# Performance work log

Hardware: AMD Instinct MI355X
Metric: run time of the kernel (lower is better)

## Reference

```python
import jax, jax.numpy as jnp
import numpy as np

H = 8          # num_channels (heads)
POS = 16       # pos_dim
MAX_F = 16.0
MIN_F = 1.0
HALF_S = 16    # samples_per_dim=32 -> offsets -16..16, S=33
SCALE = POS ** -0.5


def setup_inputs() -> dict:
    key = jax.random.key(0)
    ks = jax.random.split(key, 12)
    B, L, C = 2, 4096, 1024
    p = 0.02
    return {
        'x': jax.random.normal(ks[0], (B, L, C), jnp.float32),
        'wave_w': jax.random.normal(ks[1], (C, 3 * H), jnp.float32) * p,
        'wave_b': jax.random.normal(ks[2], (3 * H,), jnp.float32) * p,
        'query_w': jax.random.normal(ks[3], (C, H * POS), jnp.float32) * p,
        'query_b': jax.random.normal(ks[4], (H * POS,), jnp.float32) * p,
        'key_w': jax.random.normal(ks[5], (POS,), jnp.float32) * p,
        'out_w': jax.random.normal(ks[6], (C, C), jnp.float32) * p,
        'se1_w': jax.random.normal(ks[7], (C, C // 4), jnp.float32) * p,
        'se1_b': jax.random.normal(ks[8], (C // 4,), jnp.float32) * p,
        'se2_w': jax.random.normal(ks[9], (C // 4, C), jnp.float32) * p,
        'se2_b': jax.random.normal(ks[10], (C,), jnp.float32) * p,
    }


def _adaptive_conv(x, wave_w, wave_b, query_w, query_b, key_w, out_w,
                   se1_w, se1_b, se2_w, se2_b):
    B, L, C = x.shape
    D = C // H
    silu = jax.nn.silu
    offsets = jnp.arange(-HALF_S, HALF_S + 1, dtype=x.dtype)  # [S]
    S = offsets.shape[0]

    # wave params -> freq/phase/decay per (B,L,H)
    wave = silu(x @ wave_w + wave_b).reshape(B, L, 3, H)
    freq = jax.nn.sigmoid(wave[:, :, 0, :]) * (MAX_F - MIN_F) + MIN_F
    phase = jnp.tanh(wave[:, :, 1, :]) * MAX_F
    decay = jax.nn.sigmoid(wave[:, :, 2, :]) * 9.5 + 0.5
    queries = silu(x @ query_w + query_b).reshape(B, L, H, POS)

    freq_avg = freq.mean(axis=-1)    # [B,L]
    phase_avg = phase.mean(axis=-1)  # [B,L]

    centers = jnp.arange(L, dtype=x.dtype)
    # [B,L,S] real-valued sample positions
    sample_pos = (centers[None, :, None]
                  + offsets[None, None, :] * freq_avg[..., None]
                  + phase_avg[..., None])
    valid = (sample_pos >= 0) & (sample_pos < L)           # [B,L,S]
    sample_idx = jnp.clip(sample_pos.astype(jnp.int32), 0, L - 1)

    # gather: values[b,l,s,:] = x[b, sample_idx[b,l,s], :]
    values = jnp.take_along_axis(x, sample_idx.reshape(B, L * S, 1), axis=1)
    values = values.reshape(B, L, S, H, D).transpose(0, 1, 3, 2, 4)  # [B,L,H,S,D]

    rel = jnp.abs(offsets)[None, None, None, :] * freq[..., None]    # [B,L,H,S]
    keys = silu(rel[..., None] * key_w)                              # [B,L,H,S,POS]
    logits = jnp.einsum('blhd,blhsd->blhs', queries, keys) * SCALE

    vmask = valid[:, :, None, :]                                     # [B,L,H,S]
    logits = jnp.where(vmask, logits, -1e30)
    env = jnp.exp(-rel / jnp.maximum(decay[..., None], 0.1))
    w = jax.nn.softmax(logits, axis=-1) * env * vmask.astype(x.dtype)
    w = w / (w.sum(axis=-1, keepdims=True) + 1e-8)

    out = jnp.einsum('blhsd,blhs->blhd', values, w).reshape(B, L, C)
    se = jax.nn.sigmoid(silu(out @ se1_w + se1_b) @ se2_w + se2_b)
    out = out * se
    return silu(out @ out_w)


def reference(x, wave_w, wave_b, query_w, query_b, key_w, out_w,
              se1_w, se1_b, se2_w, se2_b):
    return _adaptive_conv(x, wave_w, wave_b, query_w, query_b, key_w,
                          out_w, se1_w, se1_b, se2_w, se2_b)
```

## Files before the change

kernel.cpp:

```cpp
#include <hip/hip_runtime.h>
#include <math.h>

#define HN 8
#define POSN 16
#define SN 33
#define HALF_SN 16
#define CDIM 1024
#define LDIM 4096
#define BDIM 2
#define NTOK (BDIM * LDIM)

typedef unsigned short u16;
typedef short short8 __attribute__((ext_vector_type(8)));
typedef u16 u16x8 __attribute__((ext_vector_type(8)));
typedef unsigned int u32x4 __attribute__((ext_vector_type(4)));
typedef float f32x4 __attribute__((ext_vector_type(4)));

__device__ __forceinline__ float sigf(float x) { return 1.0f / (1.0f + expf(-x)); }
__device__ __forceinline__ float siluf(float x) { return x / (1.0f + expf(-x)); }
__device__ __forceinline__ float frcp(float x) { return __builtin_amdgcn_rcpf(x); }
__device__ __forceinline__ float fexp(float x) { return __expf(x); }
__device__ __forceinline__ float fsig(float x) { return frcp(1.0f + fexp(-x)); }
__device__ __forceinline__ float fsilu(float x) { return x * fsig(x); }

__device__ __forceinline__ u16 f2b(float f) {
    union { float f; unsigned u; } v; v.f = f;
    unsigned r = v.u + 0x7fffu + ((v.u >> 16) & 1u);
    return (u16)(r >> 16);
}
__device__ __forceinline__ float b2f(u16 v) {
    union { unsigned u; float f; } x; x.u = ((unsigned)v) << 16; return x.f;
}
__device__ __forceinline__ float u2f(unsigned u) {
    union { unsigned u; float f; } x; x.u = u; return x.f;
}
__device__ __forceinline__ void ld_lds16(const void* g, void* l) {
    __builtin_amdgcn_global_load_lds(
        (const __attribute__((address_space(1))) void*)g,
        (__attribute__((address_space(3))) void*)l, 16, 0, 0);
}

__global__ __launch_bounds__(256) void transcast_all(
    const float* __restrict__ qw, const float* __restrict__ s1,
    const float* __restrict__ s2, const float* __restrict__ ow,
    const float* __restrict__ ww,
    u16* __restrict__ oq, u16* __restrict__ o1,
    u16* __restrict__ o2, u16* __restrict__ oo,
    float* __restrict__ owT)
{
    const int bid = blockIdx.x;
    if (bid >= 1664) {
        const int idx = (bid - 1664) * 256 + threadIdx.x;
        const int c = idx >> 10, k = idx & 1023;
        owT[idx] = ww[k * 24 + c];
        return;
    }
    const float* in; u16* out; int N, K, base;
    if      (bid < 128) { in = qw; out = oq; N = 128;  K = 1024; base = 0;   }
    else if (bid < 384) { in = s1; out = o1; N = 256;  K = 1024; base = 128; }
    else if (bid < 640) { in = s2; out = o2; N = 1024; K = 256;  base = 384; }
    else                { in = ow; out = oo; N = 1024; K = 1024; base = 640; }
    const int rel = bid - base, nx = N / 32;
    const int bn = (rel % nx) * 32, bk = (rel / nx) * 32;

    __shared__ float tile[32][33];
    const int tx = threadIdx.x & 31, ty = threadIdx.x >> 5;
    #pragma unroll
    for (int yy = ty; yy < 32; yy += 8)
        tile[yy][tx] = in[(size_t)(bk + yy) * N + bn + tx];
    __syncthreads();
    #pragma unroll
    for (int yy = ty; yy < 32; yy += 8)
        out[(size_t)(bn + yy) * K + bk + tx] = f2b(tile[tx][yy]);
}

__global__ __launch_bounds__(256) void wave_partial(
    const float* __restrict__ x, const float* __restrict__ wwT,
    u16* __restrict__ xbf, float* __restrict__ part)
{
    const int bid = blockIdx.x;
    const int sl = bid >> 7;
    const int tg = bid & 127;
    const int tid = threadIdx.x;
    const int t0 = tg * 64;
    const int k0 = sl * 128;

    __shared__ float wsct[24][128];

    for (int i = tid; i < 768; i += 256) {
        const int c = i >> 5, k4 = (i & 31) * 4;
        *(float4*)&wsct[c][k4] = *(const float4*)(wwT + (size_t)c * 1024 + k0 + k4);
    }
    for (int i = tid; i < 1024; i += 256) {
        const int r = i >> 4, c8 = (i & 15) * 8;
        const float* src = x + (size_t)(t0 + r) * CDIM + k0 + c8;
        float4 a = *(const float4*)(src);
        float4 b = *(const float4*)(src + 4);
        u16x8 o;
        o[0]=f2b(a.x); o[1]=f2b(a.y); o[2]=f2b(a.z); o[3]=f2b(a.w);
        o[4]=f2b(b.x); o[5]=f2b(b.y); o[6]=f2b(b.z); o[7]=f2b(b.w);
        *(u16x8*)(xbf + (size_t)(t0 + r) * CDIM + k0 + c8) = o;
    }
    __syncthreads();

    const int tok = tid & 63;
    const int cg  = tid >> 6;
    const int t = t0 + tok;
    const float* xr = x + (size_t)t * CDIM + k0;
    const int c0 = cg * 6;
    float a0=0.f, a1=0.f, a2=0.f, a3=0.f, a4=0.f, a5=0.f;

    #pragma unroll 4
    for (int kk = 0; kk < 128; kk += 4) {
        float4 xv = *(const float4*)(xr + kk);
        float4 w0 = *(const float4*)&wsct[c0 + 0][kk];
        float4 w1 = *(const float4*)&wsct[c0 + 1][kk];
        float4 w2 = *(const float4*)&wsct[c0 + 2][kk];
        float4 w3 = *(const float4*)&wsct[c0 + 3][kk];
        float4 w4 = *(const float4*)&wsct[c0 + 4][kk];
        float4 w5 = *(const float4*)&wsct[c0 + 5][kk];
        a0 += xv.x*w0.x; a0 += xv.y*w0.y; a0 += xv.z*w0.z; a0 += xv.w*w0.w;
        a1 += xv.x*w1.x; a1 += xv.y*w1.y; a1 += xv.z*w1.z; a1 += xv.w*w1.w;
        a2 += xv.x*w2.x; a2 += xv.y*w2.y; a2 += xv.z*w2.z; a2 += xv.w*w2.w;
        a3 += xv.x*w3.x; a3 += xv.y*w3.y; a3 += xv.z*w3.z; a3 += xv.w*w3.w;
        a4 += xv.x*w4.x; a4 += xv.y*w4.y; a4 += xv.z*w4.z; a4 += xv.w*w4.w;
        a5 += xv.x*w5.x; a5 += xv.y*w5.y; a5 += xv.z*w5.z; a5 += xv.w*w5.w;
    }
    float* pp = part + (size_t)sl * NTOK * 24 + (size_t)t * 24 + c0;
    pp[0]=a0; pp[1]=a1; pp[2]=a2; pp[3]=a3; pp[4]=a4; pp[5]=a5;
}

__global__ __launch_bounds__(256) void wave_fixup(
    const float* __restrict__ part, const float* __restrict__ wave_b,
    float* __restrict__ freq, float* __restrict__ decay,
    float* __restrict__ favg, float* __restrict__ pavg)
{
    const int tid = threadIdx.x;
    const int tok = tid >> 5, col = tid & 31;
    const int t = blockIdx.x * 8 + tok;
    __shared__ float fsh[8][9], psh[8][9];

    if (col < 24) {
        float s = wave_b[col];
        #pragma unroll
        for (int sl = 0; sl < 8; ++sl)
            s += part[(size_t)sl * NTOK * 24 + (size_t)t * 24 + col];
        const float val = siluf(s);
        if (col < 8) {
            float f = sigf(val) * 15.0f + 1.0f;
            freq[(size_t)t * HN + col] = f;
            fsh[tok][col] = f;
        } else if (col < 16) {
            psh[tok][col - 8] = tanhf(val) * 16.0f;
        } else {
            decay[(size_t)t * HN + (col - 16)] = sigf(val) * 9.5f + 0.5f;
        }
    }
    __syncthreads();
    if (col == 0) {
        float fa = 0.f, pa = 0.f;
        for (int h = 0; h < HN; ++h) { fa += fsh[tok][h]; pa += psh[tok][h]; }
        favg[t] = fa * 0.125f; pavg[t] = pa * 0.125f;
    }
}

template <int MODE, int CFG>
__global__ __launch_bounds__(256) void mfma_gemm(
    const u16* __restrict__ A, const u16* __restrict__ Bt,
    const float* __restrict__ bias, const u16* __restrict__ mulb,
    void* __restrict__ Cptr, int M, int N, int K)
{
    constexpr int BM  = (CFG == 0) ? 128 : 32;
    constexpr int MI  = (CFG == 0) ? 4 : 2;
    constexpr int NJ  = (CFG == 0) ? 4 : 2;
    constexpr int ACH = BM / 16;
    constexpr int NCH = ACH + 8;

    __shared__ u16 lds[2][(BM + 128) * 32];

    const int nwg = gridDim.x * gridDim.y;
    const int flat = blockIdx.y * gridDim.x + blockIdx.x;
    const int swz = (flat & 7) * (nwg >> 3) + (flat >> 3);
    const int bxi = swz / gridDim.y, byi = swz % gridDim.y;

    const int tid = threadIdx.x;
    const int bm = bxi * BM, bn = byi * 128;
    const int wid = tid >> 6, lane = tid & 63;
    const int wr = (CFG == 0) ? (wid >> 1) * 64 : 0;
    const int wc = (CFG == 0) ? (wid & 1) * 64 : wid * 32;
    const int fm = lane & 15;
    const int kg = (lane >> 4) * 8;
    const int lrow = lane >> 2;
    const int lk   = (lane & 3) * 8;

    f32x4 acc[MI][NJ];
    #pragma unroll
    for (int i = 0; i < MI; ++i)
        #pragma unroll
        for (int j = 0; j < NJ; ++j) acc[i][j] = (f32x4){0.f, 0.f, 0.f, 0.f};

    auto stage = [&](u16* dst, int k0s) {
        #pragma unroll
        for (int c = wid; c < NCH; c += 4) {
            const u16* gsrc = (c < ACH)
                ? A  + (size_t)(bm + c * 16 + lrow) * K + k0s + lk
                : Bt + (size_t)(bn + (c - ACH) * 16 + lrow) * K + k0s + lk;
            ld_lds16(gsrc, dst + c * 512 + lane * 8);
        }
    };

    stage(&lds[0][0], 0);
    __syncthreads();
    int cur = 0;
    for (int k0 = 0; k0 < K; k0 += 32) {
        const int k1 = (k0 + 32 < K) ? (k0 + 32) : k0;
        stage(&lds[cur ^ 1][0], k1);
        short8 a[MI], b[NJ];
        #pragma unroll
        for (int i = 0; i < MI; ++i)
            a[i] = *(const short8*)&lds[cur][(wr + i * 16 + fm) * 32 + kg];
        #pragma unroll
        for (int j = 0; j < NJ; ++j)
            b[j] = *(const short8*)&lds[cur][(BM + wc + j * 16 + fm) * 32 + kg];
        #pragma unroll
        for (int i = 0; i < MI; ++i)
            #pragma unroll
            for (int j = 0; j < NJ; ++j)
                acc[i][j] = __builtin_amdgcn_mfma_f32_16x16x32_bf16(a[i], b[j], acc[i][j], 0, 0, 0);
        __syncthreads();
        cur ^= 1;
    }

    float* Cf = (float*)Cptr;
    u16* Cb = (u16*)Cptr;
    #pragma unroll
    for (int i = 0; i < MI; ++i) {
        const int row0 = bm + wr + i * 16 + (lane >> 4) * 4;
        #pragma unroll
        for (int j = 0; j < NJ; ++j) {
            const int col = bn + wc + j * 16 + fm;
            const float vb = (MODE == 3) ? 0.0f : bias[col];
            #pragma unroll
            for (int e = 0; e < 4; ++e) {
                const int row = row0 + e;
                float v = acc[i][j][e];
                if (MODE == 1) v = fsilu(v + vb);
                if (MODE == 2) v = fsig(v + vb) * b2f(mulb[(size_t)row * N + col]);
                if (MODE == 3) v = fsilu(v);
                if (MODE == 3) Cf[(size_t)row * N + col] = v;
                else           Cb[(size_t)row * N + col] = f2b(v);
            }
        }
    }
}

__global__ __launch_bounds__(256) void adaptconv_kernel(
    const u16* __restrict__ xbf, const float* __restrict__ key_w,
    const u16* __restrict__ qb, const float* __restrict__ freq,
    const float* __restrict__ decay, const float* __restrict__ favg,
    const float* __restrict__ pavg, u16* __restrict__ out)
{
    const int bid = blockIdx.x;
    const int swz = (bid & 7) * (NTOK / 16) + (bid >> 3);
    const int sub = threadIdx.x >> 7, lt = threadIdx.x & 127;
    const int t = swz * 2 + sub;
    const int b = t / LDIM, l = t % LDIM;
    const int h = lt >> 4;
    const int li = lt & 15;

    __shared__ float qs[2][HN][17];
    __shared__ float kw[POSN];
    __shared__ float fr[2][HN], dc[2][HN];
    __shared__ int   boff[2][SN];
    __shared__ float msk[2][SN];
    __shared__ float vsh[2][HN][17];
    __shared__ float esh[2][HN][17];
    __shared__ float wgt[2][HN][SN];

    qs[sub][lt >> 4][lt & 15] = b2f(qb[(size_t)t * 128 + lt]);
    if (threadIdx.x < POSN) kw[threadIdx.x] = key_w[threadIdx.x];
    if (lt < HN) {
        fr[sub][lt] = freq[(size_t)t * HN + lt];
        dc[sub][lt] = decay[(size_t)t * HN + lt];
    }
    if (lt < SN) {
        float fa = favg[t], pa = pavg[t];
        float sp = (float)l + (float)(lt - HALF_SN) * fa + pa;
        bool v = (sp >= 0.0f) && (sp < (float)LDIM);
        int si = (int)sp;
        si = min(max(si, 0), LDIM - 1);
        boff[sub][lt] = si * (CDIM * 2);
        msk[sub][lt] = v ? 1.0f : 0.0f;
    }
    __syncthreads();

    {
        const float fh = fr[sub][h];
        const float rdci = frcp(fmaxf(dc[sub][h], 0.1f));
        for (int ds = li; ds < 17; ds += 16) {
            float rel = (float)ds * fh;
            float acc = 0.0f;
            #pragma unroll
            for (int p = 0; p < POSN; ++p)
                acc += qs[sub][h][p] * fsilu(rel * kw[p]);
            vsh[sub][h][ds] = 0.25f * acc;
            esh[sub][h][ds] = fexp(-rel * rdci);
        }
    }
    __syncthreads();

    {
        const int ns = (li == 0) ? 3 : 2;
        int   sI[3] = { li, li + 16, 32 };
        float lg[3];
        #pragma unroll
        for (int k = 0; k < 3; ++k) {
            if (k < ns) {
                const int s = sI[k], ds = abs(s - 16);
                lg[k] = (msk[sub][s] != 0.0f) ? vsh[sub][h][ds] : -1e30f;
            } else lg[k] = -3.4e38f;
        }
        float m = fmaxf(lg[0], fmaxf(lg[1], lg[2]));
        #pragma unroll
        for (int d = 1; d < 16; d <<= 1) m = fmaxf(m, __shfl_xor(m, d));

        float e[3]; float ssum = 0.0f;
        #pragma unroll
        for (int k = 0; k < 3; ++k) {
            e[k] = (k < ns) ? fexp(lg[k] - m) : 0.0f;
            ssum += e[k];
        }
        #pragma unroll
        for (int d = 1; d < 16; d <<= 1) ssum += __shfl_xor(ssum, d);

        const float rss = frcp(ssum);
        float wv[3]; float wsum = 0.0f;
        #pragma unroll
        for (int k = 0; k < 3; ++k) {
            if (k < ns) {
                const int s = sI[k], ds = abs(s - 16);
                wv[k] = e[k] * rss * esh[sub][h][ds] * msk[sub][s];
            } else wv[k] = 0.0f;
            wsum += wv[k];
        }
        #pragma unroll
        for (int d = 1; d < 16; d <<= 1) wsum += __shfl_xor(wsum, d);

        const float inv = frcp(wsum + 1e-8f);
        #pragma unroll
        for (int k = 0; k < 3; ++k)
            if (k < ns) wgt[sub][h][sI[k]] = wv[k] * inv;
    }
    __syncthreads();

    const char* xbB = (const char*)(xbf + (size_t)b * LDIM * CDIM);
    const int cbyte = lt * 16;
    float a0=0,a1=0,a2=0,a3=0,a4=0,a5=0,a6=0,a7=0;

    #define GFMA(V, W) do { \
        a0 += (W) * u2f((V)[0] << 16); a1 += (W) * u2f((V)[0] & 0xffff0000u); \
        a2 += (W) * u2f((V)[1] << 16); a3 += (W) * u2f((V)[1] & 0xffff0000u); \
        a4 += (W) * u2f((V)[2] << 16); a5 += (W) * u2f((V)[2] & 0xffff0000u); \
        a6 += (W) * u2f((V)[3] << 16); a7 += (W) * u2f((V)[3] & 0xffff0000u); } while (0)

    int s = 0;
    for (; s + 4 <= SN; s += 4) {
        u32x4 v0 = *(const u32x4*)(xbB + boff[sub][s]     + cbyte);
        u32x4 v1 = *(const u32x4*)(xbB + boff[sub][s + 1] + cbyte);
        u32x4 v2 = *(const u32x4*)(xbB + boff[sub][s + 2] + cbyte);
        u32x4 v3 = *(const u32x4*)(xbB + boff[sub][s + 3] + cbyte);
        float w0 = wgt[sub][h][s],     w1 = wgt[sub][h][s + 1];
        float w2 = wgt[sub][h][s + 2], w3 = wgt[sub][h][s + 3];
        GFMA(v0, w0); GFMA(v1, w1); GFMA(v2, w2); GFMA(v3, w3);
    }
    for (; s < SN; ++s) {
        u32x4 v = *(const u32x4*)(xbB + boff[sub][s] + cbyte);
        float w = wgt[sub][h][s];
        GFMA(v, w);
    }
    #undef GFMA

    u16x8 o;
    o[0]=f2b(a0); o[1]=f2b(a1); o[2]=f2b(a2); o[3]=f2b(a3);
    o[4]=f2b(a4); o[5]=f2b(a5); o[6]=f2b(a6); o[7]=f2b(a7);
    *(u16x8*)(out + (size_t)t * CDIM + lt * 8) = o;
}

extern "C" void kernel_launch(void* const* d_in, const int* in_sizes, int n_in,
                              void* d_out, int out_size, void* d_ws, size_t ws_size,
                              hipStream_t stream)
{
    const float* x       = (const float*)d_in[0];
    const float* wave_w  = (const float*)d_in[1];
    const float* wave_b  = (const float*)d_in[2];
    const float* query_w = (const float*)d_in[3];
    const float* query_b = (const float*)d_in[4];
    const float* key_w   = (const float*)d_in[5];
    const float* out_w   = (const float*)d_in[6];
    const float* se1_w   = (const float*)d_in[7];
    const float* se1_b   = (const float*)d_in[8];
    const float* se2_w   = (const float*)d_in[9];
    const float* se2_b   = (const float*)d_in[10];

    char* wsb = (char*)d_ws;
    u16* q_bf    = (u16*)wsb;           wsb += (size_t)NTOK * 128 * 2;
    float* freq  = (float*)wsb;         wsb += (size_t)NTOK * HN * 4;
    float* decay = (float*)wsb;         wsb += (size_t)NTOK * HN * 4;
    float* favg  = (float*)wsb;         wsb += (size_t)NTOK * 4;
    float* pavg  = (float*)wsb;         wsb += (size_t)NTOK * 4;
    u16* x_bf    = (u16*)wsb;           wsb += (size_t)NTOK * CDIM * 2;
    u16* conv_bf = (u16*)wsb;           wsb += (size_t)NTOK * CDIM * 2;
    u16* tmp1_bf = (u16*)wsb;           wsb += (size_t)NTOK * 256 * 2;
    u16* g_bf    = (u16*)wsb;           wsb += (size_t)NTOK * CDIM * 2;
    u16* qw_bf   = (u16*)wsb;           wsb += (size_t)128 * CDIM * 2;
    u16* se1w_bf = (u16*)wsb;           wsb += (size_t)256 * CDIM * 2;
    u16* se2w_bf = (u16*)wsb;           wsb += (size_t)CDIM * 256 * 2;
    u16* outw_bf = (u16*)wsb;           wsb += (size_t)CDIM * CDIM * 2;
    float* wwT   = (float*)wsb;         wsb += (size_t)24 * CDIM * 4;
    float* part  = (float*)wsb;         wsb += (size_t)8 * NTOK * 24 * 4;

    transcast_all<<<1760, 256, 0, stream>>>(
        query_w, se1_w, se2_w, out_w, wave_w,
        qw_bf, se1w_bf, se2w_bf, outw_bf, wwT);

    wave_partial<<<8 * 128, 256, 0, stream>>>(x, wwT, x_bf, part);
    wave_fixup<<<NTOK / 8, 256, 0, stream>>>(
        part, wave_b, freq, decay, favg, pavg);

    mfma_gemm<1, 1><<<dim3(NTOK / 32, 1), 256, 0, stream>>>(
        x_bf, qw_bf, query_b, nullptr, q_bf, NTOK, 128, CDIM);

    adaptconv_kernel<<<NTOK / 2, 256, 0, stream>>>(
        x_bf, key_w, q_bf, freq, decay, favg, pavg, conv_bf);

    mfma_gemm<1, 1><<<dim3(NTOK / 32, 256 / 128), 256, 0, stream>>>(
        conv_bf, se1w_bf, se1_b, nullptr, tmp1_bf, NTOK, 256, CDIM);

    mfma_gemm<2, 0><<<dim3(NTOK / 128, CDIM / 128), 256, 0, stream>>>(
        tmp1_bf, se2w_bf, se2_b, conv_bf, g_bf, NTOK, CDIM, 256);

    mfma_gemm<3, 0><<<dim3(NTOK / 128, CDIM / 128), 256, 0, stream>>>(
        g_bf, outw_bf, nullptr, nullptr, d_out, NTOK, CDIM, CDIM);
}
```

Measured before the change: 135.0 us.

## Fuse wave fixup into adaptconv kernel and enlarge small-GEMM tiles to 64 rows

Removes the separate wave_fixup launch and its freq/decay/avg buffers. The adaptive-conv kernel now reduces the partial wave sums itself and derives freq, phase, decay and their averages in shared memory, at the cost of two extra block barriers. The narrow-N GEMMs (query projection and SE1) switch to a 64-row tile with a 2x2 warp layout and 4 N-fragments per warp. This halves their block count and increases per-block reuse, but lowers occupancy on those launches.

```diff
diff --git a/kernel.cpp b/kernel.cpp
--- a/kernel.cpp
+++ b/kernel.cpp
@@ -130,49 +130,15 @@
     pp[0]=a0; pp[1]=a1; pp[2]=a2; pp[3]=a3; pp[4]=a4; pp[5]=a5;
 }
 
-__global__ __launch_bounds__(256) void wave_fixup(
-    const float* __restrict__ part, const float* __restrict__ wave_b,
-    float* __restrict__ freq, float* __restrict__ decay,
-    float* __restrict__ favg, float* __restrict__ pavg)
-{
-    const int tid = threadIdx.x;
-    const int tok = tid >> 5, col = tid & 31;
-    const int t = blockIdx.x * 8 + tok;
-    __shared__ float fsh[8][9], psh[8][9];
-
-    if (col < 24) {
-        float s = wave_b[col];
-        #pragma unroll
-        for (int sl = 0; sl < 8; ++sl)
-            s += part[(size_t)sl * NTOK * 24 + (size_t)t * 24 + col];
-        const float val = siluf(s);
-        if (col < 8) {
-            float f = sigf(val) * 15.0f + 1.0f;
-            freq[(size_t)t * HN + col] = f;
-            fsh[tok][col] = f;
-        } else if (col < 16) {
-            psh[tok][col - 8] = tanhf(val) * 16.0f;
-        } else {
-            decay[(size_t)t * HN + (col - 16)] = sigf(val) * 9.5f + 0.5f;
-        }
-    }
-    __syncthreads();
-    if (col == 0) {
-        float fa = 0.f, pa = 0.f;
-        for (int h = 0; h < HN; ++h) { fa += fsh[tok][h]; pa += psh[tok][h]; }
-        favg[t] = fa * 0.125f; pavg[t] = pa * 0.125f;
-    }
-}
-
 template <int MODE, int CFG>
 __global__ __launch_bounds__(256) void mfma_gemm(
     const u16* __restrict__ A, const u16* __restrict__ Bt,
     const float* __restrict__ bias, const u16* __restrict__ mulb,
     void* __restrict__ Cptr, int M, int N, int K)
 {
-    constexpr int BM  = (CFG == 0) ? 128 : 32;
+    constexpr int BM  = (CFG == 0) ? 128 : 64;
     constexpr int MI  = (CFG == 0) ? 4 : 2;
-    constexpr int NJ  = (CFG == 0) ? 4 : 2;
+    constexpr int NJ  = 4;
     constexpr int ACH = BM / 16;
     constexpr int NCH = ACH + 8;
 
@@ -186,8 +152,8 @@
     const int tid = threadIdx.x;
     const int bm = bxi * BM, bn = byi * 128;
     const int wid = tid >> 6, lane = tid & 63;
-    const int wr = (CFG == 0) ? (wid >> 1) * 64 : 0;
-    const int wc = (CFG == 0) ? (wid & 1) * 64 : wid * 32;
+    const int wr = (CFG == 0) ? (wid >> 1) * 64 : (wid >> 1) * 32;
+    const int wc = (wid & 1) * 64;
     const int fm = lane & 15;
     const int kg = (lane >> 4) * 8;
     const int lrow = lane >> 2;
@@ -256,9 +222,8 @@
 
 __global__ __launch_bounds__(256) void adaptconv_kernel(
     const u16* __restrict__ xbf, const float* __restrict__ key_w,
-    const u16* __restrict__ qb, const float* __restrict__ freq,
-    const float* __restrict__ decay, const float* __restrict__ favg,
-    const float* __restrict__ pavg, u16* __restrict__ out)
+    const u16* __restrict__ qb, const float* __restrict__ part,
+    const float* __restrict__ wave_b, u16* __restrict__ out)
 {
     const int bid = blockIdx.x;
     const int swz = (bid & 7) * (NTOK / 16) + (bid >> 3);
@@ -270,6 +235,9 @@
 
     __shared__ float qs[2][HN][17];
     __shared__ float kw[POSN];
+    __shared__ float wpre[2][24];
+    __shared__ float psh_s[2][HN];
+    __shared__ float favg_s[2], pavg_s[2];
     __shared__ float fr[2][HN], dc[2][HN];
     __shared__ int   boff[2][SN];
     __shared__ float msk[2][SN];
@@ -279,12 +247,30 @@
 
     qs[sub][lt >> 4][lt & 15] = b2f(qb[(size_t)t * 128 + lt]);
     if (threadIdx.x < POSN) kw[threadIdx.x] = key_w[threadIdx.x];
+
+    if (lt < 24) {
+        float s = wave_b[lt];
+        #pragma unroll
+        for (int sl = 0; sl < 8; ++sl)
+            s += part[(size_t)sl * NTOK * 24 + (size_t)t * 24 + lt];
+        wpre[sub][lt] = siluf(s);
+    }
+    __syncthreads();
     if (lt < HN) {
-        fr[sub][lt] = freq[(size_t)t * HN + lt];
-        dc[sub][lt] = decay[(size_t)t * HN + lt];
-    }
+        float f = sigf(wpre[sub][lt])      * 15.0f + 1.0f;
+        float p = tanhf(wpre[sub][8 + lt]) * 16.0f;
+        float d = sigf(wpre[sub][16 + lt]) * 9.5f + 0.5f;
+        fr[sub][lt] = f; dc[sub][lt] = d; psh_s[sub][lt] = p;
+    }
+    __syncthreads();
+    if (lt == 0) {
+        float fa = 0.f, pa = 0.f;
+        for (int hh = 0; hh < HN; ++hh) { fa += fr[sub][hh]; pa += psh_s[sub][hh]; }
+        favg_s[sub] = fa * 0.125f; pavg_s[sub] = pa * 0.125f;
+    }
+    __syncthreads();
     if (lt < SN) {
-        float fa = favg[t], pa = pavg[t];
+        float fa = favg_s[sub], pa = pavg_s[sub];
         float sp = (float)l + (float)(lt - HALF_SN) * fa + pa;
         bool v = (sp >= 0.0f) && (sp < (float)LDIM);
         int si = (int)sp;
@@ -404,10 +390,6 @@
 
     char* wsb = (char*)d_ws;
     u16* q_bf    = (u16*)wsb;           wsb += (size_t)NTOK * 128 * 2;
-    float* freq  = (float*)wsb;         wsb += (size_t)NTOK * HN * 4;
-    float* decay = (float*)wsb;         wsb += (size_t)NTOK * HN * 4;
-    float* favg  = (float*)wsb;         wsb += (size_t)NTOK * 4;
-    float* pavg  = (float*)wsb;         wsb += (size_t)NTOK * 4;
     u16* x_bf    = (u16*)wsb;           wsb += (size_t)NTOK * CDIM * 2;
     u16* conv_bf = (u16*)wsb;           wsb += (size_t)NTOK * CDIM * 2;
     u16* tmp1_bf = (u16*)wsb;           wsb += (size_t)NTOK * 256 * 2;
@@ -424,16 +406,14 @@
         qw_bf, se1w_bf, se2w_bf, outw_bf, wwT);
 
     wave_partial<<<8 * 128, 256, 0, stream>>>(x, wwT, x_bf, part);
-    wave_fixup<<<NTOK / 8, 256, 0, stream>>>(
-        part, wave_b, freq, decay, favg, pavg);
-
-    mfma_gemm<1, 1><<<dim3(NTOK / 32, 1), 256, 0, stream>>>(
+
+    mfma_gemm<1, 2><<<dim3(NTOK / 64, 1), 256, 0, stream>>>(
         x_bf, qw_bf, query_b, nullptr, q_bf, NTOK, 128, CDIM);
 
     adaptconv_kernel<<<NTOK / 2, 256, 0, stream>>>(
-        x_bf, key_w, q_bf, freq, decay, favg, pavg, conv_bf);
-
-    mfma_gemm<1, 1><<<dim3(NTOK / 32, 256 / 128), 256, 0, stream>>>(
+        x_bf, key_w, q_bf, part, wave_b, conv_bf);
+
+    mfma_gemm<1, 2><<<dim3(NTOK / 64, 256 / 128), 256, 0, stream>>>(
         conv_bf, se1w_bf, se1_b, nullptr, tmp1_bf, NTOK, 256, CDIM);
 
     mfma_gemm<2, 0><<<dim3(NTOK / 128, CDIM / 128), 256, 0, stream>>>(
```

New measurement: 134.7 us (median of 2 runs). No clear change (-0.2%).
